# Kernel optimization log

Measured on AMD Instinct MI355X. Metric: run time of the kernel, lower is better.

The kernel has to match this reference:

```python
import jax, jax.numpy as jnp
import numpy as np

T, D, E, INTER, TOP_K = 512, 1024, 64, 512, 4


def setup_inputs() -> dict:
    key = jax.random.key(0)
    k1, k2, k3, k4, k5 = jax.random.split(key, 5)
    s = 1.0 / np.sqrt(D)
    return {
        "hidden_states": jax.random.normal(k1, (T, D), dtype=jnp.float32),
        "gate_w": jax.random.normal(k2, (E, D), dtype=jnp.float32) * s,      # MoEGate.weight
        "w_gate": jax.random.normal(k3, (E, INTER, D), dtype=jnp.float32) * s,  # gate_proj per expert
        "w_up": jax.random.normal(k4, (E, INTER, D), dtype=jnp.float32) * s,    # up_proj per expert
        "w_down": jax.random.normal(k5, (E, D, INTER), dtype=jnp.float32) * (1.0 / np.sqrt(INTER)),  # down_proj
    }


def _moe_forward(x, gate_w, w_gate, w_up, w_down):
    # Router: logits -> softmax -> top-k -> renormalize (Qwen path of select_experts)
    logits = x @ gate_w.T                                  # [T, E]
    probs = jax.nn.softmax(logits, axis=-1)
    topk_w, topk_ids = jax.lax.top_k(probs, TOP_K)          # [T, K]
    topk_w = topk_w / jnp.sum(topk_w, axis=-1, keepdims=True)  # renormalize (norm_topk_prob)
    # Combine weights as sparse [T, E] matrix (identity logical->physical mapping)
    t_idx = jnp.arange(x.shape[0])[:, None]
    combine = jnp.zeros((x.shape[0], gate_w.shape[0]), dtype=x.dtype).at[t_idx, topk_ids].add(topk_w)
    # Expert FFN (SwiGLU), dense-over-experts reference for grouped GEMM dispatch
    g = jnp.einsum("td,efd->etf", x, w_gate)               # [E, T, INTER]
    u = jnp.einsum("td,efd->etf", x, w_up)
    h = jax.nn.silu(g) * u
    y = jnp.einsum("etf,edf->etd", h, w_down)              # [E, T, D]
    out = jnp.einsum("te,etd->td", combine, y)             # weighted combine
    return out


def reference(hidden_states, gate_w, w_gate, w_up, w_down):
    return _moe_forward(hidden_states, gate_w, w_gate, w_up, w_down)
```

## Files before the change

### kernel.cpp

```cpp
#include <hip/hip_runtime.h>
#include <hip/hip_bf16.h>
#include <cstddef>

#define T_TOK 512
#define D_DIM 1024
#define E_EXP 64
#define INTER 512
#define TOPK 4

__device__ __forceinline__ void async16(float4* ldsdst, const float* g) {
  __builtin_amdgcn_global_load_lds(
      (const __attribute__((address_space(1))) void*)g,
      (__attribute__((address_space(3))) void*)ldsdst, 16, 0, 0);
}

__global__ __launch_bounds__(64) void router_kernel(
    const float* __restrict__ x, const float* __restrict__ gate_w,
    int* __restrict__ cnt, int* __restrict__ list, float* __restrict__ pairw) {
  const int t = blockIdx.x;
  const int e = threadIdx.x;
  const float4* xr = (const float4*)(x + (size_t)t * D_DIM);
  const float4* gr = (const float4*)(gate_w + (size_t)e * D_DIM);
  float acc = 0.f;
#pragma unroll 8
  for (int i = 0; i < D_DIM / 4; i++) {
    float4 a = xr[i], b = gr[i];
    acc += a.x * b.x + a.y * b.y + a.z * b.z + a.w * b.w;
  }
  float m = acc;
  for (int off = 32; off; off >>= 1) m = fmaxf(m, __shfl_xor(m, off, 64));
  float p = __expf(acc - m);
  float s = p;
  for (int off = 32; off; off >>= 1) s += __shfl_xor(s, off, 64);
  float prob = p / s;

  float val = prob;
  int ids[TOPK];
  float ws[TOPK];
  float wsum = 0.f;
#pragma unroll
  for (int k = 0; k < TOPK; k++) {
    float v = val;
    int idx = e;
    for (int off = 32; off; off >>= 1) {
      float ov = __shfl_xor(v, off, 64);
      int oi = __shfl_xor(idx, off, 64);
      if (ov > v || (ov == v && oi < idx)) { v = ov; idx = oi; }
    }
    ids[k] = idx;
    ws[k] = v;
    wsum += v;
    if (e == idx) val = -1.f;
  }
  if (e < TOPK) {
    const int k = e;
    const int ex = ids[k];
    const float w = ws[k] / wsum;
    const int p_id = t * TOPK + k;
    pairw[p_id] = w;
    const int pos = atomicAdd(&cnt[ex], 1);
    list[ex * T_TOK + pos] = p_id;
  }
}

#define BF1 32
#define BT1 64
#define BK1 64
__global__ __launch_bounds__(256) void stage1_kernel(
    const float* __restrict__ x, const float* __restrict__ w_gate,
    const float* __restrict__ w_up, const int* __restrict__ cnt,
    const int* __restrict__ list, const float* __restrict__ pairw,
    float* __restrict__ h) {
  const int e = blockIdx.x;
  const int fbase = blockIdx.y * BF1;
  const int n = cnt[e];
  if (n == 0) return;
  __shared__ float4 lds[2][2048];
  const int tid = threadIdx.x;
  const int w = tid >> 6;
  const int lane = tid & 63;
  const int f0 = tid & 15;
  const int t0 = tid >> 4;
  const float* Wg = w_gate + ((size_t)e * INTER + fbase) * D_DIM;
  const float* Wu = w_up + ((size_t)e * INTER + fbase) * D_DIM;
  const int* mylist = list + e * T_TOK;

  int woff[8];
#pragma unroll
  for (int r = 0; r < 8; r++) {
    const int idx = r * 64 + lane;
    const int row = idx >> 4;
    const int col = (idx & 15) ^ (row & 7);
    woff[r] = row * D_DIM + 4 * col;
  }

  for (int tb = 0; tb < n; tb += BT1) {
    const float* xp[8];
    if (w >= 2) {
#pragma unroll
      for (int r = 0; r < 8; r++) {
        const int c = (w - 2) * 8 + r;
        const int idx = c * 64 + lane;
        const int row = idx >> 4;
        const int col = (idx & 15) ^ (row & 7);
        const int slot = tb + row;
        const int pid = mylist[slot < n ? slot : 0];
        xp[r] = x + (size_t)(pid >> 2) * D_DIM + 4 * col;
      }
    }
    auto stage = [&](int buf, int kb) {
      float4* B = &lds[buf][0];
      if (w == 0) {
#pragma unroll
        for (int r = 0; r < 8; r++) async16(B + r * 64, Wg + woff[r] + kb);
      } else if (w == 1) {
#pragma unroll
        for (int r = 0; r < 8; r++) async16(B + 512 + r * 64, Wu + woff[r] + kb);
      } else {
        const int c0 = (w - 2) * 8;
#pragma unroll
        for (int r = 0; r < 8; r++)
          async16(B + 1024 + (c0 + r) * 64, xp[r] + kb);
      }
    };

    float accg[2][4], accu[2][4];
#pragma unroll
    for (int i = 0; i < 2; i++)
#pragma unroll
      for (int j = 0; j < 4; j++) { accg[i][j] = 0.f; accu[i][j] = 0.f; }

    stage(0, 0);
    for (int ki = 0; ki < D_DIM / BK1; ki++) {
      __syncthreads();
      if (ki + 1 < D_DIM / BK1) stage((ki + 1) & 1, (ki + 1) * BK1);
      const float4* wgb = &lds[ki & 1][0];
      const float4* wub = wgb + 512;
      const float4* xtb = wgb + 1024;
#pragma unroll
      for (int k4 = 0; k4 < 16; k4++) {
        float4 wgv[2], wuv[2], xv[4];
#pragma unroll
        for (int i = 0; i < 2; i++) {
          const int off = (f0 + 16 * i) * 16 + (k4 ^ (f0 & 7));
          wgv[i] = wgb[off];
          wuv[i] = wub[off];
        }
#pragma unroll
        for (int j = 0; j < 4; j++)
          xv[j] = xtb[(t0 + 16 * j) * 16 + (k4 ^ (t0 & 7))];
#pragma unroll
        for (int kk = 0; kk < 4; kk++) {
#pragma unroll
          for (int i = 0; i < 2; i++) {
            const float a = ((const float*)&wgv[i])[kk];
            const float b = ((const float*)&wuv[i])[kk];
#pragma unroll
            for (int j = 0; j < 4; j++) {
              const float xx = ((const float*)&xv[j])[kk];
              accg[i][j] += a * xx;
              accu[i][j] += b * xx;
            }
          }
        }
      }
    }
#pragma unroll
    for (int j = 0; j < 4; j++) {
      const int slot = tb + t0 + 16 * j;
      if (slot < n) {
        const int pid = mylist[slot];
        const float wp = pairw[pid];
        float* hp = h + (size_t)pid * INTER + fbase;
#pragma unroll
        for (int i = 0; i < 2; i++) {
          const float g = accg[i][j];
          const float u = accu[i][j];
          hp[f0 + 16 * i] = wp * (g / (1.f + __expf(-g))) * u;
        }
      }
    }
  }
}

#define BF2 64
#define BT2 64
#define BK2 64
__global__ __launch_bounds__(256) void stage2_kernel(
    const float* __restrict__ w_down, const int* __restrict__ cnt,
    const int* __restrict__ list, const float* __restrict__ h,
    float* __restrict__ out) {
  const int e = blockIdx.x;
  const int dbase = blockIdx.y * BF2;
  const int n = cnt[e];
  if (n == 0) return;
  __shared__ float4 lds[2][2048];
  const int tid = threadIdx.x;
  const int w = tid >> 6;
  const int lane = tid & 63;
  const int d0 = tid & 15;
  const int t0 = tid >> 4;
  const float* Wd = w_down + ((size_t)e * D_DIM + dbase) * INTER;
  const int* mylist = list + e * T_TOK;

  int woff[8];
  if (w < 2) {
#pragma unroll
    for (int r = 0; r < 8; r++) {
      const int c = w * 8 + r;
      const int idx = c * 64 + lane;
      const int row = idx >> 4;
      const int col = (idx & 15) ^ (row & 7);
      woff[r] = row * INTER + 4 * col;
    }
  }

  for (int tb = 0; tb < n; tb += BT2) {
    const float* hp8[8];
    if (w >= 2) {
#pragma unroll
      for (int r = 0; r < 8; r++) {
        const int c = (w - 2) * 8 + r;
        const int idx = c * 64 + lane;
        const int row = idx >> 4;
        const int col = (idx & 15) ^ (row & 7);
        const int slot = tb + row;
        const int pid = mylist[slot < n ? slot : 0];
        hp8[r] = h + (size_t)pid * INTER + 4 * col;
      }
    }
    auto stage = [&](int buf, int kb) {
      float4* B = &lds[buf][0];
      if (w < 2) {
        const int c0 = w * 8;
#pragma unroll
        for (int r = 0; r < 8; r++)
          async16(B + (c0 + r) * 64, Wd + woff[r] + kb);
      } else {
        const int c0 = (w - 2) * 8;
#pragma unroll
        for (int r = 0; r < 8; r++)
          async16(B + 1024 + (c0 + r) * 64, hp8[r] + kb);
      }
    };

    float acc[4][4];
#pragma unroll
    for (int i = 0; i < 4; i++)
#pragma unroll
      for (int j = 0; j < 4; j++) acc[i][j] = 0.f;

    stage(0, 0);
    for (int ki = 0; ki < INTER / BK2; ki++) {
      __syncthreads();
      if (ki + 1 < INTER / BK2) stage((ki + 1) & 1, (ki + 1) * BK2);
      const float4* wdb = &lds[ki & 1][0];
      const float4* htb = wdb + 1024;
#pragma unroll
      for (int k4 = 0; k4 < 16; k4++) {
        float4 wv[4], hv[4];
#pragma unroll
        for (int i = 0; i < 4; i++)
          wv[i] = wdb[(d0 + 16 * i) * 16 + (k4 ^ (d0 & 7))];
#pragma unroll
        for (int j = 0; j < 4; j++)
          hv[j] = htb[(t0 + 16 * j) * 16 + (k4 ^ (t0 & 7))];
#pragma unroll
        for (int kk = 0; kk < 4; kk++) {
#pragma unroll
          for (int i = 0; i < 4; i++) {
            const float a = ((const float*)&wv[i])[kk];
#pragma unroll
            for (int j = 0; j < 4; j++)
              acc[i][j] += a * ((const float*)&hv[j])[kk];
          }
        }
      }
    }
#pragma unroll
    for (int j = 0; j < 4; j++) {
      const int slot = tb + t0 + 16 * j;
      if (slot < n) {
        const int tok = mylist[slot] >> 2;
        float* op = out + (size_t)tok * D_DIM + dbase;
#pragma unroll
        for (int i = 0; i < 4; i++)
          atomicAdd(&op[d0 + 16 * i], acc[i][j]);
      }
    }
  }
}

extern "C" void kernel_launch(void* const* d_in, const int* in_sizes, int n_in,
                              void* d_out, int out_size, void* d_ws, size_t ws_size,
                              hipStream_t stream) {
  const float* x = (const float*)d_in[0];
  const float* gate_w = (const float*)d_in[1];
  const float* w_gate = (const float*)d_in[2];
  const float* w_up = (const float*)d_in[3];
  const float* w_down = (const float*)d_in[4];
  float* out = (float*)d_out;

  char* ws = (char*)d_ws;
  int* cnt = (int*)ws;
  int* list = (int*)(ws + 256);
  float* pairw = (float*)(ws + 256 + E_EXP * T_TOK * 4);
  float* h = (float*)(ws + 256 + E_EXP * T_TOK * 4 + T_TOK * TOPK * 4);

  hipMemsetAsync(cnt, 0, E_EXP * sizeof(int), stream);
  hipMemsetAsync(out, 0, (size_t)T_TOK * D_DIM * sizeof(float), stream);

  router_kernel<<<T_TOK, 64, 0, stream>>>(x, gate_w, cnt, list, pairw);
  stage1_kernel<<<dim3(E_EXP, INTER / BF1), 256, 0, stream>>>(
      x, w_gate, w_up, cnt, list, pairw, h);
  stage2_kernel<<<dim3(E_EXP, D_DIM / BF2), 256, 0, stream>>>(
      w_down, cnt, list, h, out);
}
```

Before: 513.5 us.

## Use split-bf16 MFMA (hi/lo, three products) for both expert GEMMs

Replaces the scalar fp32 FMA inner loops of both expert GEMM stages with bf16 MFMA 16x16x32 instructions. Each fp32 operand is split into hi and lo bf16 parts, and three products are summed to keep accuracy close to fp32. The router now also writes split bf16 copies of x, stage1 emits h as hi/lo bf16, and weights are loaded to registers, converted and written to LDS each K-step. The goal is to move the work onto matrix cores, at the cost of 3x MFMA work, conversion overhead and some precision loss.

```diff
diff --git a/kernel.cpp b/kernel.cpp
--- a/kernel.cpp
+++ b/kernel.cpp
@@ -1,5 +1,4 @@
 #include <hip/hip_runtime.h>
-#include <hip/hip_bf16.h>
 #include <cstddef>
 
 #define T_TOK 512
@@ -8,15 +7,31 @@
 #define INTER 512
 #define TOPK 4
 
-__device__ __forceinline__ void async16(float4* ldsdst, const float* g) {
+typedef __bf16 bf16x8 __attribute__((ext_vector_type(8)));
+typedef __bf16 bf16x4 __attribute__((ext_vector_type(4)));
+typedef float f32x4 __attribute__((ext_vector_type(4)));
+
+__device__ __forceinline__ void async16(float4* ldsdst, const void* g) {
   __builtin_amdgcn_global_load_lds(
       (const __attribute__((address_space(1))) void*)g,
       (__attribute__((address_space(3))) void*)ldsdst, 16, 0, 0);
 }
 
+__device__ __forceinline__ void cvt_split8(const float4 a, const float4 b,
+                                           bf16x8& h, bf16x8& l) {
+  float f[8] = {a.x, a.y, a.z, a.w, b.x, b.y, b.z, b.w};
+#pragma unroll
+  for (int i = 0; i < 8; i++) {
+    const __bf16 hv = (__bf16)f[i];
+    h[i] = hv;
+    l[i] = (__bf16)(f[i] - (float)hv);
+  }
+}
+
 __global__ __launch_bounds__(64) void router_kernel(
     const float* __restrict__ x, const float* __restrict__ gate_w,
-    int* __restrict__ cnt, int* __restrict__ list, float* __restrict__ pairw) {
+    int* __restrict__ cnt, int* __restrict__ list, float* __restrict__ pairw,
+    __bf16* __restrict__ x_hi, __bf16* __restrict__ x_lo) {
   const int t = blockIdx.x;
   const int e = threadIdx.x;
   const float4* xr = (const float4*)(x + (size_t)t * D_DIM);
@@ -27,6 +42,15 @@
     float4 a = xr[i], b = gr[i];
     acc += a.x * b.x + a.y * b.y + a.z * b.z + a.w * b.w;
   }
+  {
+    bf16x8 h0, l0, h1, l1;
+    cvt_split8(xr[e * 4 + 0], xr[e * 4 + 1], h0, l0);
+    cvt_split8(xr[e * 4 + 2], xr[e * 4 + 3], h1, l1);
+    __bf16* xh = x_hi + (size_t)t * D_DIM + e * 16;
+    __bf16* xl = x_lo + (size_t)t * D_DIM + e * 16;
+    *(bf16x8*)(xh) = h0; *(bf16x8*)(xh + 8) = h1;
+    *(bf16x8*)(xl) = l0; *(bf16x8*)(xl + 8) = l1;
+  }
   float m = acc;
   for (int off = 32; off; off >>= 1) m = fmaxf(m, __shfl_xor(m, off, 64));
   float p = __expf(acc - m);
@@ -65,12 +89,13 @@
 
 #define BF1 32
 #define BT1 64
-#define BK1 64
+#define NK1 (D_DIM / 64)
 __global__ __launch_bounds__(256) void stage1_kernel(
-    const float* __restrict__ x, const float* __restrict__ w_gate,
-    const float* __restrict__ w_up, const int* __restrict__ cnt,
-    const int* __restrict__ list, const float* __restrict__ pairw,
-    float* __restrict__ h) {
+    const __bf16* __restrict__ x_hi, const __bf16* __restrict__ x_lo,
+    const float* __restrict__ w_gate, const float* __restrict__ w_up,
+    const int* __restrict__ cnt, const int* __restrict__ list,
+    const float* __restrict__ pairw,
+    __bf16* __restrict__ h_hi, __bf16* __restrict__ h_lo) {
   const int e = blockIdx.x;
   const int fbase = blockIdx.y * BF1;
   const int n = cnt[e];
@@ -79,117 +104,121 @@
   const int tid = threadIdx.x;
   const int w = tid >> 6;
   const int lane = tid & 63;
-  const int f0 = tid & 15;
-  const int t0 = tid >> 4;
-  const float* Wg = w_gate + ((size_t)e * INTER + fbase) * D_DIM;
-  const float* Wu = w_up + ((size_t)e * INTER + fbase) * D_DIM;
+  const int lrow = lane & 15;
+  const int lk = lane >> 4;
   const int* mylist = list + e * T_TOK;
 
-  int woff[8];
-#pragma unroll
-  for (int r = 0; r < 8; r++) {
-    const int idx = r * 64 + lane;
-    const int row = idx >> 4;
-    const int col = (idx & 15) ^ (row & 7);
-    woff[r] = row * D_DIM + 4 * col;
-  }
+  const int wrow = tid >> 3;
+  const int wblk = tid & 7;
+  const float* gsrc = w_gate + ((size_t)e * INTER + fbase + wrow) * D_DIM + wblk * 8;
+  const float* usrc = w_up + ((size_t)e * INTER + fbase + wrow) * D_DIM + wblk * 8;
+  const int wunit = wrow * 8 + (wblk ^ (wrow & 7));
+
+  float4 wreg[4];
 
   for (int tb = 0; tb < n; tb += BT1) {
-    const float* xp[8];
-    if (w >= 2) {
-#pragma unroll
-      for (int r = 0; r < 8; r++) {
-        const int c = (w - 2) * 8 + r;
-        const int idx = c * 64 + lane;
-        const int row = idx >> 4;
-        const int col = (idx & 15) ^ (row & 7);
-        const int slot = tb + row;
-        const int pid = mylist[slot < n ? slot : 0];
-        xp[r] = x + (size_t)(pid >> 2) * D_DIM + 4 * col;
-      }
-    }
-    auto stage = [&](int buf, int kb) {
+    const __bf16* xsrc[4];
+#pragma unroll
+    for (int r = 0; r < 4; r++) {
+      const int u = w * 256 + r * 64 + lane;
+      const int uu = u & 511;
+      const int row = uu >> 3;
+      const int blk = (uu & 7) ^ (row & 7);
+      const int slot = tb + row;
+      const int pid = mylist[slot < n ? slot : 0];
+      const __bf16* base = (u < 512) ? x_hi : x_lo;
+      xsrc[r] = base + (size_t)(pid >> 2) * D_DIM + blk * 8;
+    }
+
+    auto stage_load = [&](int buf, int kb) {
+      const float4* g4 = (const float4*)(gsrc + kb);
+      const float4* u4 = (const float4*)(usrc + kb);
+      wreg[0] = g4[0]; wreg[1] = g4[1];
+      wreg[2] = u4[0]; wreg[3] = u4[1];
       float4* B = &lds[buf][0];
-      if (w == 0) {
-#pragma unroll
-        for (int r = 0; r < 8; r++) async16(B + r * 64, Wg + woff[r] + kb);
-      } else if (w == 1) {
-#pragma unroll
-        for (int r = 0; r < 8; r++) async16(B + 512 + r * 64, Wu + woff[r] + kb);
-      } else {
-        const int c0 = (w - 2) * 8;
-#pragma unroll
-        for (int r = 0; r < 8; r++)
-          async16(B + 1024 + (c0 + r) * 64, xp[r] + kb);
-      }
+#pragma unroll
+      for (int r = 0; r < 4; r++)
+        async16(B + 1024 + w * 256 + r * 64, xsrc[r] + kb);
     };
-
-    float accg[2][4], accu[2][4];
-#pragma unroll
-    for (int i = 0; i < 2; i++)
-#pragma unroll
-      for (int j = 0; j < 4; j++) { accg[i][j] = 0.f; accu[i][j] = 0.f; }
-
-    stage(0, 0);
-    for (int ki = 0; ki < D_DIM / BK1; ki++) {
+    auto convert_write = [&](int buf) {
+      __bf16* L = (__bf16*)&lds[buf][0];
+      bf16x8 h0, l0;
+      cvt_split8(wreg[0], wreg[1], h0, l0);
+      *(bf16x8*)(L + (size_t)wunit * 8) = h0;
+      *(bf16x8*)(L + (size_t)(wunit + 256) * 8) = l0;
+      cvt_split8(wreg[2], wreg[3], h0, l0);
+      *(bf16x8*)(L + (size_t)(wunit + 512) * 8) = h0;
+      *(bf16x8*)(L + (size_t)(wunit + 768) * 8) = l0;
+    };
+
+    f32x4 accg[2] = {};
+    f32x4 accu[2] = {};
+    const bool active = (tb + w * 16) < n;
+
+    stage_load(0, 0);
+    convert_write(0);
+    for (int ki = 0; ki < NK1; ki++) {
       __syncthreads();
-      if (ki + 1 < D_DIM / BK1) stage((ki + 1) & 1, (ki + 1) * BK1);
-      const float4* wgb = &lds[ki & 1][0];
-      const float4* wub = wgb + 512;
-      const float4* xtb = wgb + 1024;
-#pragma unroll
-      for (int k4 = 0; k4 < 16; k4++) {
-        float4 wgv[2], wuv[2], xv[4];
-#pragma unroll
-        for (int i = 0; i < 2; i++) {
-          const int off = (f0 + 16 * i) * 16 + (k4 ^ (f0 & 7));
-          wgv[i] = wgb[off];
-          wuv[i] = wub[off];
-        }
-#pragma unroll
-        for (int j = 0; j < 4; j++)
-          xv[j] = xtb[(t0 + 16 * j) * 16 + (k4 ^ (t0 & 7))];
-#pragma unroll
-        for (int kk = 0; kk < 4; kk++) {
+      if (ki + 1 < NK1) stage_load((ki + 1) & 1, (ki + 1) * 64);
+      if (active) {
+        const __bf16* L = (const __bf16*)&lds[ki & 1][0];
+#pragma unroll
+        for (int s = 0; s < 2; s++) {
+          const int blk = s * 4 + lk;
+          const int xr = w * 16 + lrow;
+          const int xu = xr * 8 + (blk ^ (xr & 7));
+          const bf16x8 xh = *(const bf16x8*)(L + (size_t)(1024 + xu) * 8);
+          const bf16x8 xl = *(const bf16x8*)(L + (size_t)(1536 + xu) * 8);
 #pragma unroll
           for (int i = 0; i < 2; i++) {
-            const float a = ((const float*)&wgv[i])[kk];
-            const float b = ((const float*)&wuv[i])[kk];
-#pragma unroll
-            for (int j = 0; j < 4; j++) {
-              const float xx = ((const float*)&xv[j])[kk];
-              accg[i][j] += a * xx;
-              accu[i][j] += b * xx;
-            }
+            const int fr = i * 16 + lrow;
+            const int fu = fr * 8 + (blk ^ (fr & 7));
+            const bf16x8 gh = *(const bf16x8*)(L + (size_t)fu * 8);
+            const bf16x8 gl = *(const bf16x8*)(L + (size_t)(256 + fu) * 8);
+            const bf16x8 uh = *(const bf16x8*)(L + (size_t)(512 + fu) * 8);
+            const bf16x8 ul = *(const bf16x8*)(L + (size_t)(768 + fu) * 8);
+            accg[i] = __builtin_amdgcn_mfma_f32_16x16x32_bf16(gh, xh, accg[i], 0, 0, 0);
+            accg[i] = __builtin_amdgcn_mfma_f32_16x16x32_bf16(gh, xl, accg[i], 0, 0, 0);
+            accg[i] = __builtin_amdgcn_mfma_f32_16x16x32_bf16(gl, xh, accg[i], 0, 0, 0);
+            accu[i] = __builtin_amdgcn_mfma_f32_16x16x32_bf16(uh, xh, accu[i], 0, 0, 0);
+            accu[i] = __builtin_amdgcn_mfma_f32_16x16x32_bf16(uh, xl, accu[i], 0, 0, 0);
+            accu[i] = __builtin_amdgcn_mfma_f32_16x16x32_bf16(ul, xh, accu[i], 0, 0, 0);
           }
         }
       }
-    }
-#pragma unroll
-    for (int j = 0; j < 4; j++) {
-      const int slot = tb + t0 + 16 * j;
-      if (slot < n) {
-        const int pid = mylist[slot];
-        const float wp = pairw[pid];
-        float* hp = h + (size_t)pid * INTER + fbase;
-#pragma unroll
-        for (int i = 0; i < 2; i++) {
-          const float g = accg[i][j];
-          const float u = accu[i][j];
-          hp[f0 + 16 * i] = wp * (g / (1.f + __expf(-g))) * u;
+      if (ki + 1 < NK1) convert_write((ki + 1) & 1);
+    }
+    const int slot = tb + w * 16 + lrow;
+    if (slot < n) {
+      const int pid = mylist[slot];
+      const float wp = pairw[pid];
+      __bf16* hh = h_hi + (size_t)pid * INTER + fbase;
+      __bf16* hl = h_lo + (size_t)pid * INTER + fbase;
+#pragma unroll
+      for (int i = 0; i < 2; i++) {
+        bf16x4 vh, vl;
+#pragma unroll
+        for (int r = 0; r < 4; r++) {
+          const float g = accg[i][r];
+          const float u = accu[i][r];
+          const float v = wp * (g / (1.f + __expf(-g))) * u;
+          const __bf16 hv = (__bf16)v;
+          vh[r] = hv;
+          vl[r] = (__bf16)(v - (float)hv);
         }
+        *(bf16x4*)(hh + i * 16 + lk * 4) = vh;
+        *(bf16x4*)(hl + i * 16 + lk * 4) = vl;
       }
     }
   }
 }
 
 #define BF2 64
-#define BT2 64
-#define BK2 64
+#define NK2 (INTER / 64)
 __global__ __launch_bounds__(256) void stage2_kernel(
     const float* __restrict__ w_down, const int* __restrict__ cnt,
-    const int* __restrict__ list, const float* __restrict__ h,
-    float* __restrict__ out) {
+    const int* __restrict__ list, const __bf16* __restrict__ h_hi,
+    const __bf16* __restrict__ h_lo, float* __restrict__ out) {
   const int e = blockIdx.x;
   const int dbase = blockIdx.y * BF2;
   const int n = cnt[e];
@@ -198,94 +227,94 @@
   const int tid = threadIdx.x;
   const int w = tid >> 6;
   const int lane = tid & 63;
-  const int d0 = tid & 15;
-  const int t0 = tid >> 4;
-  const float* Wd = w_down + ((size_t)e * D_DIM + dbase) * INTER;
+  const int lrow = lane & 15;
+  const int lk = lane >> 4;
   const int* mylist = list + e * T_TOK;
 
-  int woff[8];
-  if (w < 2) {
-#pragma unroll
-    for (int r = 0; r < 8; r++) {
-      const int c = w * 8 + r;
-      const int idx = c * 64 + lane;
-      const int row = idx >> 4;
-      const int col = (idx & 15) ^ (row & 7);
-      woff[r] = row * INTER + 4 * col;
-    }
-  }
-
-  for (int tb = 0; tb < n; tb += BT2) {
-    const float* hp8[8];
-    if (w >= 2) {
-#pragma unroll
-      for (int r = 0; r < 8; r++) {
-        const int c = (w - 2) * 8 + r;
-        const int idx = c * 64 + lane;
-        const int row = idx >> 4;
-        const int col = (idx & 15) ^ (row & 7);
-        const int slot = tb + row;
-        const int pid = mylist[slot < n ? slot : 0];
-        hp8[r] = h + (size_t)pid * INTER + 4 * col;
-      }
-    }
-    auto stage = [&](int buf, int kb) {
+  const int wrow = tid >> 3;
+  const int wblk = tid & 7;
+  const float* dsrc0 = w_down + ((size_t)e * D_DIM + dbase + wrow) * INTER + wblk * 8;
+  const float* dsrc1 = w_down + ((size_t)e * D_DIM + dbase + wrow + 32) * INTER + wblk * 8;
+  const int wunit0 = wrow * 8 + (wblk ^ (wrow & 7));
+  const int wunit1 = wunit0 + 256;
+
+  float4 wreg[4];
+
+  for (int tb = 0; tb < n; tb += BT1) {
+    const __bf16* hsrc[4];
+#pragma unroll
+    for (int r = 0; r < 4; r++) {
+      const int u = w * 256 + r * 64 + lane;
+      const int uu = u & 511;
+      const int row = uu >> 3;
+      const int blk = (uu & 7) ^ (row & 7);
+      const int slot = tb + row;
+      const int pid = mylist[slot < n ? slot : 0];
+      const __bf16* base = (u < 512) ? h_hi : h_lo;
+      hsrc[r] = base + (size_t)pid * INTER + blk * 8;
+    }
+
+    auto stage_load = [&](int buf, int kb) {
+      const float4* a4 = (const float4*)(dsrc0 + kb);
+      const float4* b4 = (const float4*)(dsrc1 + kb);
+      wreg[0] = a4[0]; wreg[1] = a4[1];
+      wreg[2] = b4[0]; wreg[3] = b4[1];
       float4* B = &lds[buf][0];
-      if (w < 2) {
-        const int c0 = w * 8;
-#pragma unroll
-        for (int r = 0; r < 8; r++)
-          async16(B + (c0 + r) * 64, Wd + woff[r] + kb);
-      } else {
-        const int c0 = (w - 2) * 8;
-#pragma unroll
-        for (int r = 0; r < 8; r++)
-          async16(B + 1024 + (c0 + r) * 64, hp8[r] + kb);
-      }
+#pragma unroll
+      for (int r = 0; r < 4; r++)
+        async16(B + 1024 + w * 256 + r * 64, hsrc[r] + kb);
     };
-
-    float acc[4][4];
-#pragma unroll
-    for (int i = 0; i < 4; i++)
-#pragma unroll
-      for (int j = 0; j < 4; j++) acc[i][j] = 0.f;
-
-    stage(0, 0);
-    for (int ki = 0; ki < INTER / BK2; ki++) {
+    auto convert_write = [&](int buf) {
+      __bf16* L = (__bf16*)&lds[buf][0];
+      bf16x8 h0, l0;
+      cvt_split8(wreg[0], wreg[1], h0, l0);
+      *(bf16x8*)(L + (size_t)wunit0 * 8) = h0;
+      *(bf16x8*)(L + (size_t)(wunit0 + 512) * 8) = l0;
+      cvt_split8(wreg[2], wreg[3], h0, l0);
+      *(bf16x8*)(L + (size_t)wunit1 * 8) = h0;
+      *(bf16x8*)(L + (size_t)(wunit1 + 512) * 8) = l0;
+    };
+
+    f32x4 acc[4] = {};
+    const bool active = (tb + w * 16) < n;
+
+    stage_load(0, 0);
+    convert_write(0);
+    for (int ki = 0; ki < NK2; ki++) {
       __syncthreads();
-      if (ki + 1 < INTER / BK2) stage((ki + 1) & 1, (ki + 1) * BK2);
-      const float4* wdb = &lds[ki & 1][0];
-      const float4* htb = wdb + 1024;
-#pragma unroll
-      for (int k4 = 0; k4 < 16; k4++) {
-        float4 wv[4], hv[4];
-#pragma unroll
-        for (int i = 0; i < 4; i++)
-          wv[i] = wdb[(d0 + 16 * i) * 16 + (k4 ^ (d0 & 7))];
-#pragma unroll
-        for (int j = 0; j < 4; j++)
-          hv[j] = htb[(t0 + 16 * j) * 16 + (k4 ^ (t0 & 7))];
-#pragma unroll
-        for (int kk = 0; kk < 4; kk++) {
+      if (ki + 1 < NK2) stage_load((ki + 1) & 1, (ki + 1) * 64);
+      if (active) {
+        const __bf16* L = (const __bf16*)&lds[ki & 1][0];
+#pragma unroll
+        for (int s = 0; s < 2; s++) {
+          const int blk = s * 4 + lk;
+          const int hr = w * 16 + lrow;
+          const int hu = hr * 8 + (blk ^ (hr & 7));
+          const bf16x8 hh = *(const bf16x8*)(L + (size_t)(1024 + hu) * 8);
+          const bf16x8 hl = *(const bf16x8*)(L + (size_t)(1536 + hu) * 8);
 #pragma unroll
           for (int i = 0; i < 4; i++) {
-            const float a = ((const float*)&wv[i])[kk];
-#pragma unroll
-            for (int j = 0; j < 4; j++)
-              acc[i][j] += a * ((const float*)&hv[j])[kk];
+            const int dr = i * 16 + lrow;
+            const int du = dr * 8 + (blk ^ (dr & 7));
+            const bf16x8 wh = *(const bf16x8*)(L + (size_t)du * 8);
+            const bf16x8 wl = *(const bf16x8*)(L + (size_t)(512 + du) * 8);
+            acc[i] = __builtin_amdgcn_mfma_f32_16x16x32_bf16(wh, hh, acc[i], 0, 0, 0);
+            acc[i] = __builtin_amdgcn_mfma_f32_16x16x32_bf16(wh, hl, acc[i], 0, 0, 0);
+            acc[i] = __builtin_amdgcn_mfma_f32_16x16x32_bf16(wl, hh, acc[i], 0, 0, 0);
           }
         }
       }
-    }
-#pragma unroll
-    for (int j = 0; j < 4; j++) {
-      const int slot = tb + t0 + 16 * j;
-      if (slot < n) {
-        const int tok = mylist[slot] >> 2;
-        float* op = out + (size_t)tok * D_DIM + dbase;
-#pragma unroll
-        for (int i = 0; i < 4; i++)
-          atomicAdd(&op[d0 + 16 * i], acc[i][j]);
+      if (ki + 1 < NK2) convert_write((ki + 1) & 1);
+    }
+    const int slot = tb + w * 16 + lrow;
+    if (slot < n) {
+      const int tok = mylist[slot] >> 2;
+      float* op = out + (size_t)tok * D_DIM + dbase;
+#pragma unroll
+      for (int i = 0; i < 4; i++) {
+#pragma unroll
+        for (int r = 0; r < 4; r++)
+          atomicAdd(&op[i * 16 + lk * 4 + r], acc[i][r]);
       }
     }
   }
@@ -302,17 +331,21 @@
   float* out = (float*)d_out;
 
   char* ws = (char*)d_ws;
-  int* cnt = (int*)ws;
-  int* list = (int*)(ws + 256);
-  float* pairw = (float*)(ws + 256 + E_EXP * T_TOK * 4);
-  float* h = (float*)(ws + 256 + E_EXP * T_TOK * 4 + T_TOK * TOPK * 4);
+  size_t off = 0;
+  int* cnt = (int*)(ws + off); off += 256;
+  int* list = (int*)(ws + off); off += (size_t)E_EXP * T_TOK * 4;
+  float* pairw = (float*)(ws + off); off += (size_t)T_TOK * TOPK * 4;
+  __bf16* h_hi = (__bf16*)(ws + off); off += (size_t)T_TOK * TOPK * INTER * 2;
+  __bf16* h_lo = (__bf16*)(ws + off); off += (size_t)T_TOK * TOPK * INTER * 2;
+  __bf16* x_hi = (__bf16*)(ws + off); off += (size_t)T_TOK * D_DIM * 2;
+  __bf16* x_lo = (__bf16*)(ws + off); off += (size_t)T_TOK * D_DIM * 2;
 
   hipMemsetAsync(cnt, 0, E_EXP * sizeof(int), stream);
   hipMemsetAsync(out, 0, (size_t)T_TOK * D_DIM * sizeof(float), stream);
 
-  router_kernel<<<T_TOK, 64, 0, stream>>>(x, gate_w, cnt, list, pairw);
+  router_kernel<<<T_TOK, 64, 0, stream>>>(x, gate_w, cnt, list, pairw, x_hi, x_lo);
   stage1_kernel<<<dim3(E_EXP, INTER / BF1), 256, 0, stream>>>(
-      x, w_gate, w_up, cnt, list, pairw, h);
+      x_hi, x_lo, w_gate, w_up, cnt, list, pairw, h_hi, h_lo);
   stage2_kernel<<<dim3(E_EXP, D_DIM / BF2), 256, 0, stream>>>(
-      w_down, cnt, list, h, out);
-}
+      w_down, cnt, list, h_hi, h_lo, out);
+}
```

New measurement: 455.4 us. 1.13x faster.
